# Performance work log

Hardware: AMD Instinct MI355X
Metric: run time of the kernel (lower is better)

Reference implementation:

```python
import jax, jax.numpy as jnp
import numpy as np

N_Q, N_K, N_HEAD, D_HEAD = 2048, 2048, 8, 64


def setup_inputs() -> dict:
    key = jax.random.key(0)
    kq, kk, ka = jax.random.split(key, 3)
    q = jax.random.normal(kq, (N_Q, N_HEAD, D_HEAD), dtype=jnp.float32)
    k = jax.random.normal(kk, (N_K, N_HEAD, D_HEAD), dtype=jnp.float32)
    # glorot-style init for attn param of shape (1, n_head, 2*d_head)
    fan = N_HEAD * 2 * D_HEAD
    std = float(np.sqrt(6.0 / fan))
    attn = jax.random.uniform(ka, (1, N_HEAD, 2 * D_HEAD), dtype=jnp.float32,
                              minval=-std, maxval=std)
    return {"q": q, "k": k, "attn": attn}


def reference(q, k, attn):
    # attn: (1, n_head, 2*d_head) -> split into query half and key half
    d_head = q.shape[-1]
    a_q = attn[0, :, :d_head]   # (n_head, d_head)
    a_k = attn[0, :, d_head:]   # (n_head, d_head)
    # Additive score without materializing the (n_q, n_k, n_head, 2*d_head)
    # concatenated tensor: score[i,j,h] = relu(q_i_h . a_q_h + k_j_h . a_k_h)
    sq = jnp.einsum("qhd,hd->qh", q, a_q)  # (n_q, n_head)
    sk = jnp.einsum("khd,hd->kh", k, a_k)  # (n_k, n_head)
    scores = jax.nn.relu(sq[:, None, :] + sk[None, :, :])  # (n_q, n_k, n_head)
    # Faithful to original: softmax over dim=-1 at shape (n_q*n_k, n_head),
    # i.e. over the head dimension. mask=None, dropout=0.0.
    return jax.nn.softmax(scores, axis=-1)
```

## Files before the change

kernel.cpp:

```cpp
#include <hip/hip_runtime.h>
#include <hip/hip_bf16.h>


#define N_Q   2048
#define N_K   2048
#define N_HEAD 8
#define D_HEAD 64

__global__ __launch_bounds__(256) void proj_kernel(
    const float* __restrict__ q, const float* __restrict__ k,
    const float* __restrict__ attn,
    float* __restrict__ sq, float* __restrict__ sk)
{
    int tid = blockIdx.x * blockDim.x + threadIdx.x;
    int lane8 = tid & 7;
    int pair  = tid >> 3;
    const int PAIRS = N_Q * N_HEAD;
    bool is_k = pair >= PAIRS;
    int p = is_k ? (pair - PAIRS) : pair;
    int h = p & (N_HEAD - 1);

    const float* src = is_k ? k : q;
    const float* a   = attn + h * (2 * D_HEAD) + (is_k ? D_HEAD : 0);

    const float4* s4 = (const float4*)(src + (size_t)p * D_HEAD + lane8 * 8);
    const float4* a4 = (const float4*)(a + lane8 * 8);
    float4 x0 = s4[0], x1 = s4[1];
    float4 w0 = a4[0], w1 = a4[1];
    float sum = x0.x*w0.x + x0.y*w0.y + x0.z*w0.z + x0.w*w0.w
              + x1.x*w1.x + x1.y*w1.y + x1.z*w1.z + x1.w*w1.w;

    sum += __shfl_xor(sum, 1);
    sum += __shfl_xor(sum, 2);
    sum += __shfl_xor(sum, 4);

    if (lane8 == 0) {
        (is_k ? sk : sq)[p] = sum;
    }
}

__global__ __launch_bounds__(256) void softmax_kernel(
    const float* __restrict__ sq, const float* __restrict__ sk,
    float* __restrict__ out)
{
    int t = blockIdx.x * blockDim.x + threadIdx.x;
    int i = blockIdx.y;

    float4 qv = *(const float4*)(sq + i * N_HEAD + (t & 1) * 4);
    float4 kv = *(const float4*)(sk + t * 4);

    const float LOG2E = 1.4426950408889634f;
    float v0 = __builtin_amdgcn_exp2f(fmaxf(qv.x + kv.x, 0.0f) * LOG2E);
    float v1 = __builtin_amdgcn_exp2f(fmaxf(qv.y + kv.y, 0.0f) * LOG2E);
    float v2 = __builtin_amdgcn_exp2f(fmaxf(qv.z + kv.z, 0.0f) * LOG2E);
    float v3 = __builtin_amdgcn_exp2f(fmaxf(qv.w + kv.w, 0.0f) * LOG2E);

    float ps = (v0 + v1) + (v2 + v3);
    float s  = ps + __shfl_xor(ps, 1);
    float r  = __builtin_amdgcn_rcpf(s);

    float4 o = make_float4(v0 * r, v1 * r, v2 * r, v3 * r);
    *(float4*)(out + (size_t)i * N_K * N_HEAD + t * 4) = o;
}

extern "C" void kernel_launch(void* const* d_in, const int* in_sizes, int n_in,
                              void* d_out, int out_size, void* d_ws, size_t ws_size,
                              hipStream_t stream) {
    const float* q    = (const float*)d_in[0];
    const float* k    = (const float*)d_in[1];
    const float* attn = (const float*)d_in[2];
    float* out = (float*)d_out;

    float* sq = (float*)d_ws;
    float* sk = sq + N_Q * N_HEAD;

    int total_threads = 2 * N_Q * N_HEAD * 8;
    proj_kernel<<<dim3(total_threads / 256), dim3(256), 0, stream>>>(q, k, attn, sq, sk);

    softmax_kernel<<<dim3(2 * N_K / 256, N_Q), dim3(256), 0, stream>>>(sq, sk, out);
}
```

Baseline: 139.7 us.

## Use persistent grid-stride softmax blocks and fold log2e into projections

The softmax kernel now launches a fixed 2048-block grid, and each thread loops over 16 rows. Because the stride is a multiple of 4096 float4 elements, each thread keeps the same key-score float4 in a register and loads it once. The log2(e) scale moves into the projection kernel's stores, which removes one multiply per exponential. The aim is to cut block launch overhead and redundant key loads in a write-bound kernel, at the cost of fewer resident waves and a longer per-thread loop.

```diff
diff --git a/kernel.cpp b/kernel.cpp
--- a/kernel.cpp
+++ b/kernel.cpp
@@ -1,5 +1,4 @@
 #include <hip/hip_runtime.h>
-#include <hip/hip_bf16.h>
 
 
 #define N_Q   2048
@@ -35,32 +34,43 @@
     sum += __shfl_xor(sum, 4);
 
     if (lane8 == 0) {
-        (is_k ? sk : sq)[p] = sum;
+        (is_k ? sk : sq)[p] = sum * 1.4426950408889634f;
     }
 }
+
+#define SM_BLOCKS 2048
+#define SM_ITERS  16
 
 __global__ __launch_bounds__(256) void softmax_kernel(
     const float* __restrict__ sq, const float* __restrict__ sk,
     float* __restrict__ out)
 {
-    int t = blockIdx.x * blockDim.x + threadIdx.x;
-    int i = blockIdx.y;
+    const int STRIDE = SM_BLOCKS * 256;
+    int f0 = blockIdx.x * 256 + threadIdx.x;
+    int t  = f0 & (2 * N_K - 1);
+    int half = f0 & 1;
 
-    float4 qv = *(const float4*)(sq + i * N_HEAD + (t & 1) * 4);
-    float4 kv = *(const float4*)(sk + t * 4);
+    float4 kv = ((const float4*)sk)[t];
+    const float4* sq4 = (const float4*)sq;
+    float4* out4 = (float4*)out;
 
-    const float LOG2E = 1.4426950408889634f;
-    float v0 = __builtin_amdgcn_exp2f(fmaxf(qv.x + kv.x, 0.0f) * LOG2E);
-    float v1 = __builtin_amdgcn_exp2f(fmaxf(qv.y + kv.y, 0.0f) * LOG2E);
-    float v2 = __builtin_amdgcn_exp2f(fmaxf(qv.z + kv.z, 0.0f) * LOG2E);
-    float v3 = __builtin_amdgcn_exp2f(fmaxf(qv.w + kv.w, 0.0f) * LOG2E);
+    #pragma unroll
+    for (int it = 0; it < SM_ITERS; ++it) {
+        int f = f0 + it * STRIDE;
+        int i = f >> 12;
+        float4 qv = sq4[2 * i + half];
 
-    float ps = (v0 + v1) + (v2 + v3);
-    float s  = ps + __shfl_xor(ps, 1);
-    float r  = __builtin_amdgcn_rcpf(s);
+        float v0 = __builtin_amdgcn_exp2f(fmaxf(qv.x + kv.x, 0.0f));
+        float v1 = __builtin_amdgcn_exp2f(fmaxf(qv.y + kv.y, 0.0f));
+        float v2 = __builtin_amdgcn_exp2f(fmaxf(qv.z + kv.z, 0.0f));
+        float v3 = __builtin_amdgcn_exp2f(fmaxf(qv.w + kv.w, 0.0f));
 
-    float4 o = make_float4(v0 * r, v1 * r, v2 * r, v3 * r);
-    *(float4*)(out + (size_t)i * N_K * N_HEAD + t * 4) = o;
+        float ps = (v0 + v1) + (v2 + v3);
+        float s  = ps + __shfl_xor(ps, 1);
+        float r  = __builtin_amdgcn_rcpf(s);
+
+        out4[f] = make_float4(v0 * r, v1 * r, v2 * r, v3 * r);
+    }
 }
 
 extern "C" void kernel_launch(void* const* d_in, const int* in_sizes, int n_in,
@@ -77,5 +87,5 @@
     int total_threads = 2 * N_Q * N_HEAD * 8;
     proj_kernel<<<dim3(total_threads / 256), dim3(256), 0, stream>>>(q, k, attn, sq, sk);
 
-    softmax_kernel<<<dim3(2 * N_K / 256, N_Q), dim3(256), 0, stream>>>(sq, sk, out);
+    softmax_kernel<<<dim3(SM_BLOCKS), dim3(256), 0, stream>>>(sq, sk, out);
 }
```

After: 143.1 us. 1.02x slower.
